# Performance work log

Measured on AMD Instinct MI355X. Metric: run time of the kernel, lower is better.

Reference implementation:

```python
import jax, jax.numpy as jnp
import numpy as np

H, C = 8, 16          # heads, per-head dim; hidden = H*C = 128
NEG_SLOPE = 0.2       # GATConv default
EPS = 1e-5            # GraphNorm eps


def setup_inputs() -> dict:
    key = jax.random.key(0)
    ks = iter(jax.random.split(key, 64))
    Np, Na, D, E = 100000, 50000, 128, 500000
    s = 1.0 / np.sqrt(D)

    def w(shape, scale=1.0):
        return jax.random.normal(next(ks), shape, jnp.float32) * scale

    inp = {
        'x_paper': w((Np, D)),
        'x_author': w((Na, D)),
        'edge_writes': jnp.stack([
            jax.random.randint(next(ks), (E,), 0, Na),
            jax.random.randint(next(ks), (E,), 0, Np)]).astype(jnp.int32),
        'edge_cites': jnp.stack([
            jax.random.randint(next(ks), (E,), 0, Np),
            jax.random.randint(next(ks), (E,), 0, Np)]).astype(jnp.int32),
        'W_lin_paper': w((D, 128), s), 'b_lin_paper': jnp.zeros((128,), jnp.float32),
        'W_lin_author': w((D, 128), s), 'b_lin_author': jnp.zeros((128,), jnp.float32),
        'Wsrc_writes': w((128, 128), s), 'Wdst_writes': w((128, 128), s),
        'atts_writes': w((H, C), 0.1), 'attd_writes': w((H, C), 0.1),
        'bias_writes': jnp.zeros((128,), jnp.float32),
        'Wsrc_cites': w((128, 128), s), 'Wdst_cites': w((128, 128), s),
        'atts_cites': w((H, C), 0.1), 'attd_cites': w((H, C), 0.1),
        'bias_cites': jnp.zeros((128,), jnp.float32),
        'gnw_paper': jnp.ones((128,), jnp.float32), 'gnb_paper': jnp.zeros((128,), jnp.float32),
        'gnm_paper': jnp.ones((128,), jnp.float32),
        'gnw_author': jnp.ones((128,), jnp.float32), 'gnb_author': jnp.zeros((128,), jnp.float32),
        'gnm_author': jnp.ones((128,), jnp.float32),
        'W2_paper': w((128, 128), s), 'b2_paper': jnp.zeros((128,), jnp.float32),
        'W2_author': w((128, 128), s), 'b2_author': jnp.zeros((128,), jnp.float32),
    }
    return inp


def _gat(src_emb, dst_emb, ei, Wsrc, Wdst, att_s, att_d, bias, n_dst):
    # PyG GATConv, bipartite input, concat=True, add_self_loops=True (eval / no dropout)
    n_self = min(src_emb.shape[0], n_dst)
    loops = jnp.arange(n_self, dtype=ei.dtype)
    src = jnp.concatenate([ei[0], loops])
    dst = jnp.concatenate([ei[1], loops])
    xs = (src_emb @ Wsrc).reshape(-1, H, C)          # [Ns,H,C]
    xd = (dst_emb @ Wdst).reshape(-1, H, C)          # [Nd,H,C]
    a_s = (xs * att_s).sum(-1)                       # [Ns,H]
    a_d = (xd * att_d).sum(-1)                       # [Nd,H]
    e = jax.nn.leaky_relu(a_s[src] + a_d[dst], NEG_SLOPE)   # [E,H]
    m = jax.ops.segment_max(e, dst, num_segments=n_dst)
    m = jnp.where(jnp.isfinite(m), m, 0.0)           # guard empty segments
    p = jnp.exp(e - m[dst])
    denom = jax.ops.segment_sum(p, dst, num_segments=n_dst)
    alpha = p / (denom[dst] + 1e-16)                 # segment softmax over dst
    msg = xs[src] * alpha[:, :, None]                # [E,H,C]
    out = jax.ops.segment_sum(msg, dst, num_segments=n_dst)  # [Nd,H,C]
    return out.reshape(n_dst, H * C) + bias


def _gnorm(x, w, b, ms):
    mu = x.mean(0)
    o = x - ms * mu
    var = (o * o).mean(0)
    return w * o * jax.lax.rsqrt(var + EPS) + b


def reference(x_paper, x_author, edge_writes, edge_cites,
              W_lin_paper, b_lin_paper, W_lin_author, b_lin_author,
              Wsrc_writes, Wdst_writes, atts_writes, attd_writes, bias_writes,
              Wsrc_cites, Wdst_cites, atts_cites, attd_cites, bias_cites,
              gnw_paper, gnb_paper, gnm_paper, gnw_author, gnb_author, gnm_author,
              W2_paper, b2_paper, W2_author, b2_author):
    emb_p = jax.nn.relu(x_paper @ W_lin_paper + b_lin_paper)
    emb_a = jax.nn.relu(x_author @ W_lin_author + b_lin_author)
    Np = emb_p.shape[0]
    out_p = _gat(emb_a, emb_p, edge_writes, Wsrc_writes, Wdst_writes,
                 atts_writes, attd_writes, bias_writes, Np)
    out_p = out_p + _gat(emb_p, emb_p, edge_cites, Wsrc_cites, Wdst_cites,
                         atts_cites, attd_cites, bias_cites, Np)
    out_a = jnp.zeros((emb_a.shape[0], H * C), x_author.dtype)  # no edge type targets author
    out_p = _gnorm(out_p, gnw_paper, gnb_paper, gnm_paper) @ W2_paper + b2_paper
    out_a = _gnorm(out_a, gnw_author, gnb_author, gnm_author) @ W2_author + b2_author
    return (out_p, out_a)
```

## Files before the change

kernel.cpp:

```cpp
#include <hip/hip_runtime.h>
#include <cstdint>
#include <cstddef>

#define H 8
#define DHID 128
#define XST 144
#define BM 64
#define LDST 136
#define NEG_SLOPE 0.2f
#define GN_EPS 1e-5f

#define SCAN_T 256
#define SCAN_I 4

typedef __attribute__((ext_vector_type(8))) short short8;
typedef __attribute__((ext_vector_type(4))) float f32x4;

__device__ __forceinline__ void atomAddF(float* p, float v) {
    __hip_atomic_fetch_add(p, v, __ATOMIC_RELAXED, __HIP_MEMORY_SCOPE_AGENT);
}
__device__ __forceinline__ unsigned short f2bf(float f) {
    uint32_t u = __float_as_uint(f);
    uint32_t r = (u + 0x7FFFu + ((u >> 16) & 1u)) >> 16;
    return (unsigned short)r;
}
__device__ __forceinline__ uint32_t pack2bf(float lo, float hi) {
    return (uint32_t)f2bf(lo) | ((uint32_t)f2bf(hi) << 16);
}
__device__ __forceinline__ float bflo(uint32_t v) { return __uint_as_float(v << 16); }
__device__ __forceinline__ float bfhi(uint32_t v) { return __uint_as_float(v & 0xFFFF0000u); }

struct PrepHist {
    const float *Wlp, *Wsc, *Wla, *Wsw, *W2p;
    const float *Wdw, *adw, *asc_, *Wdc, *adc_, *asw_;
    unsigned short *WlinP_p, *WsrcP_c, *WlinP_a, *WsrcP_w, *W2P_p, *VscP_p, *VscP_a;
    const float *bw, *bc, *gnb_a, *W2a, *b2a;
    float *bsum, *row_a, *colsum, *colsumsq;
    unsigned short *xs_w_ph, *xs_c_ph;
    const int *dst_w, *dst_c;
    int *deg, *rank;
    int Ew, Ec, Np, HB0;
};

__global__ void prep_hist(PrepHist a) {
    int b = blockIdx.x, t = threadIdx.x;
    if (b >= a.HB0) {
        int base = (b - a.HB0) * 1024 + t;
        int E = a.Ew + a.Ec;
        int dd[4];
        bool val[4];
#pragma unroll
        for (int j = 0; j < 4; ++j) {
            int i = base + j * 256;
            val[j] = i < E;
            dd[j] = 0;
            if (val[j]) dd[j] = (i < a.Ew) ? a.dst_w[i] : (a.Np + a.dst_c[i - a.Ew]);
        }
        int rk[4];
#pragma unroll
        for (int j = 0; j < 4; ++j)
            if (val[j]) rk[j] = atomicAdd(&a.deg[dd[j]], 1);
#pragma unroll
        for (int j = 0; j < 4; ++j)
            if (val[j]) a.rank[base + j * 256] = rk[j];
        return;
    }
    if (b == 56) {
        if (t < 128) {
            a.bsum[t] = a.bw[t] + a.bc[t];
            float acc = a.b2a[t];
            for (int k = 0; k < DHID; ++k) acc += a.gnb_a[k] * a.W2a[k * DHID + t];
            a.row_a[t] = acc;
            a.colsum[t] = 0.f;
            a.colsumsq[t] = 0.f;
            a.xs_w_ph[t] = 0;
            a.xs_c_ph[t] = 0;
        } else if (t < 136) {
            *reinterpret_cast<float*>(a.xs_w_ph + 128 + 2 * (t - 128)) = -1e30f;
        } else if (t < 144) {
            *reinterpret_cast<float*>(a.xs_c_ph + 128 + 2 * (t - 136)) = -1e30f;
        }
        return;
    }
    int j = b >> 3;
    int idx = (b & 7) * 256 + t;
    int lane = idx & 63, kk = (idx >> 6) & 3, nt = idx >> 8;
    int col = nt * 16 + (lane & 15);
    int k0 = kk * 32 + ((lane >> 4) << 3);
    if (j < 5) {
        const float* W = j == 0 ? a.Wlp : j == 1 ? a.Wsc : j == 2 ? a.Wla : j == 3 ? a.Wsw : a.W2p;
        unsigned short* out = j == 0 ? a.WlinP_p : j == 1 ? a.WsrcP_c : j == 2 ? a.WlinP_a
                              : j == 3 ? a.WsrcP_w : a.W2P_p;
        for (int i = 0; i < 8; ++i) out[idx * 8 + i] = f2bf(W[(k0 + i) * DHID + col]);
    } else if (j == 5) {
        if (idx >= 2 * 256) return;
        const float *W = nullptr, *A = nullptr;
        int h = col & 7;
        if (col < 24) {
            int which = col >> 3;
            W = which == 0 ? a.Wdw : which == 1 ? a.Wsc : a.Wdc;
            A = which == 0 ? a.adw : which == 1 ? a.asc_ : a.adc_;
        }
        for (int i = 0; i < 8; ++i) {
            float v = 0.f;
            if (W)
                for (int c = 0; c < 16; ++c) v += W[(k0 + i) * DHID + h * 16 + c] * A[h * 16 + c];
            a.VscP_p[idx * 8 + i] = f2bf(v);
        }
    } else {
        if (idx >= 256) return;
        int h = col & 7;
        for (int i = 0; i < 8; ++i) {
            float v = 0.f;
            if (col < 8)
                for (int c = 0; c < 16; ++c)
                    v += a.Wsw[(k0 + i) * DHID + h * 16 + c] * a.asw_[h * 16 + c];
            a.VscP_a[idx * 8 + i] = f2bf(v);
        }
    }
}

__global__ void scan1(const int* __restrict__ in, int n, int* __restrict__ out,
                      int* __restrict__ bsums) {
    __shared__ int sh[SCAN_T];
    int t = threadIdx.x;
    long base = (long)blockIdx.x * SCAN_T * SCAN_I;
    int v[SCAN_I];
    int s = 0;
#pragma unroll
    for (int j = 0; j < SCAN_I; ++j) {
        long idx = base + (long)t * SCAN_I + j;
        int x = (idx < n) ? in[idx] : 0;
        x = (x + 3) & ~3;
        v[j] = x;
        s += x;
    }
    sh[t] = s;
    __syncthreads();
    for (int off = 1; off < SCAN_T; off <<= 1) {
        int x = (t >= off) ? sh[t - off] : 0;
        __syncthreads();
        sh[t] += x;
        __syncthreads();
    }
    int run = sh[t] - s;
#pragma unroll
    for (int j = 0; j < SCAN_I; ++j) {
        long idx = base + (long)t * SCAN_I + j;
        if (idx < n) out[idx] = run;
        run += v[j];
    }
    if (t == SCAN_T - 1) bsums[blockIdx.x] = sh[SCAN_T - 1];
}

__global__ void scan3_tails(const int* __restrict__ off_raw, const int* __restrict__ bs1,
                            int nb, int n2, int* __restrict__ off2,
                            const int* __restrict__ deg,
                            int Np, int Na, int* __restrict__ srcu) {
    __shared__ int pf[SCAN_T];
    int t = threadIdx.x;
    pf[t] = (t < nb) ? bs1[t] : 0;
    __syncthreads();
    for (int off = 1; off < SCAN_T; off <<= 1) {
        int x = (t >= off) ? pf[t - off] : 0;
        __syncthreads();
        pf[t] += x;
        __syncthreads();
    }
    int i = blockIdx.x * 256 + t;
    if (i < n2) {
        int g = i >> 10;
        int o = off_raw[i] + (g ? pf[g - 1] : 0);
        off2[i] = o;
        int dgi = deg[i];
        int padded = (dgi + 3) & ~3;
        int ph = (i < Np) ? Na : Np;
        for (int k = dgi; k < padded; ++k) srcu[o + k] = ph;
    }
    if (blockIdx.x == 0 && t == 0) off2[n2] = pf[nb - 1];
}

template <int NSC>
__device__ void proj_body(unsigned short* xt, int bid,
                          const float* __restrict__ x, int nrows,
                          const unsigned short* __restrict__ WlinP, const float* __restrict__ blin,
                          const unsigned short* __restrict__ WsrcP,
                          const unsigned short* __restrict__ VscP,
                          unsigned short* __restrict__ xs,
                          float* __restrict__ ad0, float* __restrict__ ad1) {
    int t = threadIdx.x;
    int lane = t & 63, w = t >> 6;
    long row0 = (long)bid * BM;
    for (int it = 0; it < 16; ++it) {
        int idx2 = t + it * 256;
        int r = idx2 >> 6, cp = idx2 & 63;
        long gr = row0 + r;
        float v0 = 0.f, v1 = 0.f;
        if (gr < nrows) { v0 = x[gr * DHID + 2 * cp]; v1 = x[gr * DHID + 2 * cp + 1]; }
        *reinterpret_cast<uint32_t*>(&xt[r * LDST + 2 * cp]) = pack2bf(v0, v1);
    }
    __syncthreads();
    int arow = w * 16 + (lane & 15);
    int koff = (lane >> 4) << 3;
    short8 af[4];
#pragma unroll
    for (int kk = 0; kk < 4; ++kk)
        af[kk] = *reinterpret_cast<const short8*>(&xt[arow * LDST + kk * 32 + koff]);
    const short8* Bl = reinterpret_cast<const short8*>(WlinP);
    f32x4 acc[8];
#pragma unroll
    for (int nt = 0; nt < 8; ++nt) {
        f32x4 a = {0.f, 0.f, 0.f, 0.f};
#pragma unroll
        for (int kk = 0; kk < 4; ++kk)
            a = __builtin_amdgcn_mfma_f32_16x16x32_bf16(af[kk], Bl[(nt * 4 + kk) * 64 + lane], a, 0, 0, 0);
        acc[nt] = a;
    }
    __syncthreads();
    int orow = w * 16 + ((lane >> 4) << 2);
    int ccol = lane & 15;
#pragma unroll
    for (int nt = 0; nt < 8; ++nt) {
        float b = blin[nt * 16 + ccol];
#pragma unroll
        for (int r = 0; r < 4; ++r) {
            float e = fmaxf(acc[nt][r] + b, 0.f);
            xt[(orow + r) * LDST + nt * 16 + ccol] = f2bf(e);
        }
    }
    __syncthreads();
#pragma unroll
    for (int kk = 0; kk < 4; ++kk)
        af[kk] = *reinterpret_cast<const short8*>(&xt[arow * LDST + kk * 32 + koff]);
    const short8* Bs = reinterpret_cast<const short8*>(WsrcP);
#pragma unroll
    for (int nt = 0; nt < 8; ++nt) {
        f32x4 a = {0.f, 0.f, 0.f, 0.f};
#pragma unroll
        for (int kk = 0; kk < 4; ++kk)
            a = __builtin_amdgcn_mfma_f32_16x16x32_bf16(af[kk], Bs[(nt * 4 + kk) * 64 + lane], a, 0, 0, 0);
        acc[nt] = a;
    }
    const short8* Bv = reinterpret_cast<const short8*>(VscP);
    f32x4 sacc0 = {0.f, 0.f, 0.f, 0.f}, sacc1 = {0.f, 0.f, 0.f, 0.f};
#pragma unroll
    for (int kk = 0; kk < 4; ++kk)
        sacc0 = __builtin_amdgcn_mfma_f32_16x16x32_bf16(af[kk], Bv[kk * 64 + lane], sacc0, 0, 0, 0);
    if (NSC > 1) {
#pragma unroll
        for (int kk = 0; kk < 4; ++kk)
            sacc1 = __builtin_amdgcn_mfma_f32_16x16x32_bf16(af[kk], Bv[(4 + kk) * 64 + lane], sacc1, 0, 0, 0);
    }
#pragma unroll
    for (int nt = 0; nt < 8; ++nt) {
#pragma unroll
        for (int r = 0; r < 4; ++r) {
            long gr = row0 + orow + r;
            if (gr < nrows) xs[gr * XST + nt * 16 + ccol] = f2bf(acc[nt][r]);
        }
    }
#pragma unroll
    for (int st = 0; st < NSC; ++st) {
        int scol = st * 16 + ccol;
        int h = scol & 7, which = scol >> 3;
        f32x4 s = (st == 0) ? sacc0 : sacc1;
#pragma unroll
        for (int r = 0; r < 4; ++r) {
            long gr = row0 + orow + r;
            if (gr >= nrows) continue;
            if (NSC == 2) {
                if (which == 0) ad0[gr * H + h] = s[r];
                else if (which == 1)
                    *reinterpret_cast<float*>(xs + gr * XST + 128 + 2 * h) = s[r];
                else if (which == 2) ad1[gr * H + h] = s[r];
            } else {
                if (which == 0)
                    *reinterpret_cast<float*>(xs + gr * XST + 128 + 2 * h) = s[r];
            }
        }
    }
}

struct MegaArgs {
    const float* x_p; int Np;
    const unsigned short* WlinP_p; const float* blp;
    const unsigned short* WsrcP_c; const unsigned short* VscP_p;
    unsigned short* xs_c; float *a_d_w, *a_d_c;
    const float* x_a; int Na;
    const unsigned short* WlinP_a; const float* bla;
    const unsigned short* WsrcP_w; const unsigned short* VscP_a;
    unsigned short* xs_w;
    const int *src_w, *dst_w, *src_c, *dst_c;
    int Ew, Ec;
    const int *off2, *rank;
    int* srcu;
    int PB, AB;
};

__global__ __launch_bounds__(256) void mega(MegaArgs a) {
    __shared__ unsigned short xt[BM * LDST];
    int b = blockIdx.x;
    if (b < a.PB) {
        proj_body<2>(xt, b, a.x_p, a.Np, a.WlinP_p, a.blp, a.WsrcP_c, a.VscP_p,
                     a.xs_c, a.a_d_w, a.a_d_c);
        return;
    }
    if (b < a.PB + a.AB) {
        proj_body<1>(xt, b - a.PB, a.x_a, a.Na, a.WlinP_a, a.bla, a.WsrcP_w, a.VscP_a,
                     a.xs_w, nullptr, nullptr);
        return;
    }
    int base = (b - a.PB - a.AB) * 1024 + threadIdx.x;
    int E = a.Ew + a.Ec;
    int s[4], di[4], rk[4];
    bool val[4];
#pragma unroll
    for (int j = 0; j < 4; ++j) {
        int i = base + j * 256;
        val[j] = i < E;
        s[j] = di[j] = rk[j] = 0;
        if (val[j]) {
            if (i < a.Ew) { s[j] = a.src_w[i]; di[j] = a.dst_w[i]; }
            else { int q = i - a.Ew; s[j] = a.src_c[q]; di[j] = a.Np + a.dst_c[q]; }
            rk[j] = a.rank[i];
        }
    }
    int pos[4];
#pragma unroll
    for (int j = 0; j < 4; ++j)
        if (val[j]) pos[j] = a.off2[di[j]] + rk[j];
#pragma unroll
    for (int j = 0; j < 4; ++j)
        if (val[j]) a.srcu[pos[j]] = s[j];
}

#define FILLB 391
__global__ __launch_bounds__(256) void gat_gather(
    const int* __restrict__ off, const int* __restrict__ srcu,
    const float* __restrict__ a_d_w, const float* __restrict__ a_d_c,
    const unsigned short* __restrict__ xs_w, const unsigned short* __restrict__ xs_c,
    uint32_t* __restrict__ gatb, int Np, int nselfw,
    const float* __restrict__ row_a, float4* __restrict__ outa, long n4) {
    if (blockIdx.x < FILLB) {
        long i = (long)blockIdx.x * 256 + threadIdx.x;
        long stride = (long)FILLB * 256;
        const float4* r4 = reinterpret_cast<const float4*>(row_a);
        for (; i < n4; i += stride) outa[i] = r4[i & 31];
        return;
    }
    int l = threadIdx.x & 63;
    int d = (blockIdx.x - FILLB) * 4 + (threadIdx.x >> 6);
    if (d >= Np) return;
    int h = l >> 3;
    int sco = 128 + 2 * h;
    int iw = off[d], w1 = off[d + 1];
    int ic = off[Np + d], c1 = off[Np + d + 1];
    float adw = a_d_w[(long)d * H + h];
    float adc = a_d_c[(long)d * H + h];
    float denw = 0.f, n0w = 0.f, n1w = 0.f;
    float denc = 0.f, n0c = 0.f, n1c = 0.f;
    if (d < nselfw) {
        const unsigned short* r = xs_w + (long)d * XST;
        float e = *reinterpret_cast<const float*>(r + sco) + adw;
        e = e > 0.f ? e : NEG_SLOPE * e;
        float p = __expf(e);
        uint32_t v = *reinterpret_cast<const uint32_t*>(r + 2 * l);
        denw += p; n0w += p * bflo(v); n1w += p * bfhi(v);
    }
    {
        const unsigned short* r = xs_c + (long)d * XST;
        float e = *reinterpret_cast<const float*>(r + sco) + adc;
        e = e > 0.f ? e : NEG_SLOPE * e;
        float p = __expf(e);
        uint32_t v = *reinterpret_cast<const uint32_t*>(r + 2 * l);
        denc += p; n0c += p * bflo(v); n1c += p * bfhi(v);
    }
    while (iw < w1 || ic < c1) {
        bool hw = iw < w1, hc = ic < c1;
        int4 sw, sc;
        if (hw) sw = *reinterpret_cast<const int4*>(srcu + iw);
        if (hc) sc = *reinterpret_cast<const int4*>(srcu + ic);
        float ew[4], ec[4];
        uint32_t vw[4], vc[4];
        if (hw) {
            const unsigned short* r0 = xs_w + (long)sw.x * XST;
            const unsigned short* r1 = xs_w + (long)sw.y * XST;
            const unsigned short* r2 = xs_w + (long)sw.z * XST;
            const unsigned short* r3 = xs_w + (long)sw.w * XST;
            ew[0] = *reinterpret_cast<const float*>(r0 + sco);
            ew[1] = *reinterpret_cast<const float*>(r1 + sco);
            ew[2] = *reinterpret_cast<const float*>(r2 + sco);
            ew[3] = *reinterpret_cast<const float*>(r3 + sco);
            vw[0] = *reinterpret_cast<const uint32_t*>(r0 + 2 * l);
            vw[1] = *reinterpret_cast<const uint32_t*>(r1 + 2 * l);
            vw[2] = *reinterpret_cast<const uint32_t*>(r2 + 2 * l);
            vw[3] = *reinterpret_cast<const uint32_t*>(r3 + 2 * l);
        }
        if (hc) {
            const unsigned short* r0 = xs_c + (long)sc.x * XST;
            const unsigned short* r1 = xs_c + (long)sc.y * XST;
            const unsigned short* r2 = xs_c + (long)sc.z * XST;
            const unsigned short* r3 = xs_c + (long)sc.w * XST;
            ec[0] = *reinterpret_cast<const float*>(r0 + sco);
            ec[1] = *reinterpret_cast<const float*>(r1 + sco);
            ec[2] = *reinterpret_cast<const float*>(r2 + sco);
            ec[3] = *reinterpret_cast<const float*>(r3 + sco);
            vc[0] = *reinterpret_cast<const uint32_t*>(r0 + 2 * l);
            vc[1] = *reinterpret_cast<const uint32_t*>(r1 + 2 * l);
            vc[2] = *reinterpret_cast<const uint32_t*>(r2 + 2 * l);
            vc[3] = *reinterpret_cast<const uint32_t*>(r3 + 2 * l);
        }
        if (hw) {
#pragma unroll
            for (int j = 0; j < 4; ++j) {
                float e = ew[j] + adw;
                e = e > 0.f ? e : NEG_SLOPE * e;
                float p = __expf(e);
                denw += p;
                n0w += p * bflo(vw[j]);
                n1w += p * bfhi(vw[j]);
            }
            iw += 4;
        }
        if (hc) {
#pragma unroll
            for (int j = 0; j < 4; ++j) {
                float e = ec[j] + adc;
                e = e > 0.f ? e : NEG_SLOPE * e;
                float p = __expf(e);
                denc += p;
                n0c += p * bflo(vc[j]);
                n1c += p * bfhi(vc[j]);
            }
            ic += 4;
        }
    }
    float rw = 1.f / (denw + 1e-16f);
    float rc = 1.f / (denc + 1e-16f);
    gatb[(long)d * 64 + l] = pack2bf(n0w * rw + n0c * rc, n1w * rw + n1c * rc);
}

#define GN_ROWS 512
__global__ void gn_reduce(const uint32_t* __restrict__ gatb, const float* __restrict__ bsum,
                          float* __restrict__ colsum, float* __restrict__ colsumsq, int Np) {
    int t = threadIdx.x;
    int p = t & 63, ro = t >> 6;
    long r0 = (long)blockIdx.x * GN_ROWS + ro;
    long r1 = min((long)(blockIdx.x + 1) * GN_ROWS, (long)Np);
    float b0 = bsum[2 * p], b1 = bsum[2 * p + 1];
    float s1a = 0.f, s2a = 0.f, s1b = 0.f, s2b = 0.f;
    for (long r = r0; r < r1; r += 4) {
        uint32_t u = gatb[r * 64 + p];
        float x0 = bflo(u) + b0, x1 = bfhi(u) + b1;
        s1a += x0; s2a += x0 * x0;
        s1b += x1; s2b += x1 * x1;
    }
    atomAddF(colsum + 2 * p, s1a);
    atomAddF(colsumsq + 2 * p, s2a);
    atomAddF(colsum + 2 * p + 1, s1b);
    atomAddF(colsumsq + 2 * p + 1, s2b);
}

__global__ __launch_bounds__(256) void final_fill(
    const uint32_t* __restrict__ gatb, const float* __restrict__ bsum,
    const float* __restrict__ colsum, const float* __restrict__ colsumsq,
    const float* __restrict__ gnw, const float* __restrict__ gnb,
    const float* __restrict__ gnm,
    const unsigned short* __restrict__ W2P, const float* __restrict__ b2,
    float* __restrict__ out, int Np) {
    __shared__ unsigned short xt[BM * LDST];
    __shared__ float cscale[DHID], cshift[DHID];
    int b = blockIdx.x;
    int t = threadIdx.x;
    int lane = t & 63, w = t >> 6;
    long row0 = (long)b * BM;
    if (t < DHID) {
        float invN = 1.f / (float)Np;
        float mu = colsum[t] * invN;
        float ms = gnm[t];
        float var = colsumsq[t] * invN - mu * mu * ms * (2.f - ms);
        float sc = gnw[t] * rsqrtf(var + GN_EPS);
        cscale[t] = sc;
        cshift[t] = (bsum[t] - ms * mu) * sc + gnb[t];
    }
    __syncthreads();
    int wrow0 = w * 16;
    float cs0 = cscale[2 * lane], cf0 = cshift[2 * lane];
    float cs1 = cscale[2 * lane + 1], cf1 = cshift[2 * lane + 1];
    for (int it = 0; it < 16; ++it) {
        int r = wrow0 + it;
        long gr = row0 + r;
        float v0 = 0.f, v1 = 0.f;
        if (gr < Np) {
            uint32_t u = gatb[gr * 64 + lane];
            v0 = bflo(u) * cs0 + cf0;
            v1 = bfhi(u) * cs1 + cf1;
        }
        *reinterpret_cast<uint32_t*>(&xt[r * LDST + 2 * lane]) = pack2bf(v0, v1);
    }
    int arow = wrow0 + (lane & 15);
    int koff = (lane >> 4) << 3;
    short8 af[4];
#pragma unroll
    for (int kk = 0; kk < 4; ++kk)
        af[kk] = *reinterpret_cast<const short8*>(&xt[arow * LDST + kk * 32 + koff]);
    const short8* Bw = reinterpret_cast<const short8*>(W2P);
    int orow = wrow0 + ((lane >> 4) << 2);
    int ccol = lane & 15;
#pragma unroll
    for (int nt = 0; nt < 8; ++nt) {
        f32x4 a = {0.f, 0.f, 0.f, 0.f};
#pragma unroll
        for (int kk = 0; kk < 4; ++kk)
            a = __builtin_amdgcn_mfma_f32_16x16x32_bf16(af[kk], Bw[(nt * 4 + kk) * 64 + lane], a, 0, 0, 0);
        float bb = b2[nt * 16 + ccol];
#pragma unroll
        for (int r = 0; r < 4; ++r) {
            long gr = row0 + orow + r;
            if (gr < Np) out[gr * DHID + nt * 16 + ccol] = a[r] + bb;
        }
    }
}

extern "C" void kernel_launch(void* const* d_in, const int* in_sizes, int n_in,
                              void* d_out, int out_size, void* d_ws, size_t ws_size,
                              hipStream_t stream) {
    const float* x_p   = (const float*)d_in[0];
    const float* x_a   = (const float*)d_in[1];
    const int*   e_w   = (const int*)d_in[2];
    const int*   e_c   = (const int*)d_in[3];
    const float* Wlp   = (const float*)d_in[4];
    const float* blp   = (const float*)d_in[5];
    const float* Wla   = (const float*)d_in[6];
    const float* bla   = (const float*)d_in[7];
    const float* Wsw   = (const float*)d_in[8];
    const float* Wdw   = (const float*)d_in[9];
    const float* asw   = (const float*)d_in[10];
    const float* adw   = (const float*)d_in[11];
    const float* bw    = (const float*)d_in[12];
    const float* Wsc   = (const float*)d_in[13];
    const float* Wdc   = (const float*)d_in[14];
    const float* asc   = (const float*)d_in[15];
    const float* adc   = (const float*)d_in[16];
    const float* bc    = (const float*)d_in[17];
    const float* gnw_p = (const float*)d_in[18];
    const float* gnb_p = (const float*)d_in[19];
    const float* gnm_p = (const float*)d_in[20];
    const float* gnb_a = (const float*)d_in[22];
    const float* W2p   = (const float*)d_in[24];
    const float* b2p   = (const float*)d_in[25];
    const float* W2a   = (const float*)d_in[26];
    const float* b2a   = (const float*)d_in[27];

    int Np = in_sizes[0] / DHID;
    int Na = in_sizes[1] / DHID;
    int Ew = in_sizes[2] / 2;
    int Ec = in_sizes[3] / 2;
    int nself_w = Na < Np ? Na : Np;
    int tot_edges = Ew + Ec;
    int maxTot = tot_edges + 6 * Np + 8;

    float* ws = (float*)d_ws;
    uint32_t* gatb = (uint32_t*)ws;
    float* a_d_w = (float*)(gatb + (size_t)Np * 64);
    float* a_d_c = a_d_w + (size_t)Np * H;
    float* bsum  = a_d_c + (size_t)Np * H;
    float* row_a = bsum + DHID;
    float* colsum   = row_a + DHID;
    float* colsumsq = colsum + DHID;
    int*   deg   = (int*)(colsumsq + DHID);
    int* off_raw = deg + 2 * Np;
    int* off2    = off_raw + 2 * Np;
    int* bs1     = off2 + 2 * Np + 1;
    uintptr_t up = (uintptr_t)(bs1 + 512);
    up = (up + 15) & ~(uintptr_t)15;
    int* srcu = (int*)up;
    int* rank = srcu + maxTot;
    unsigned short* xs_w = (unsigned short*)(rank + tot_edges);
    unsigned short* xs_c = xs_w + (size_t)(Na + 1) * XST;
    up = (uintptr_t)(xs_c + (size_t)(Np + 1) * XST);
    up = (up + 15) & ~(uintptr_t)15;
    unsigned short* WlinP_p = (unsigned short*)up;
    unsigned short* WsrcP_c = WlinP_p + 16384;
    unsigned short* WlinP_a = WsrcP_c + 16384;
    unsigned short* WsrcP_w = WlinP_a + 16384;
    unsigned short* W2P_p   = WsrcP_w + 16384;
    unsigned short* VscP_p  = W2P_p + 16384;
    unsigned short* VscP_a  = VscP_p + 4096;

    hipMemsetAsync(deg, 0, 2 * (size_t)Np * sizeof(int), stream);

    int HB = (tot_edges + 1023) / 1024;
    {
        PrepHist pa;
        pa.Wlp = Wlp; pa.Wsc = Wsc; pa.Wla = Wla; pa.Wsw = Wsw; pa.W2p = W2p;
        pa.Wdw = Wdw; pa.adw = adw; pa.asc_ = asc; pa.Wdc = Wdc; pa.adc_ = adc; pa.asw_ = asw;
        pa.WlinP_p = WlinP_p; pa.WsrcP_c = WsrcP_c; pa.WlinP_a = WlinP_a;
        pa.WsrcP_w = WsrcP_w; pa.W2P_p = W2P_p; pa.VscP_p = VscP_p; pa.VscP_a = VscP_a;
        pa.bw = bw; pa.bc = bc; pa.gnb_a = gnb_a; pa.W2a = W2a; pa.b2a = b2a;
        pa.bsum = bsum; pa.row_a = row_a; pa.colsum = colsum; pa.colsumsq = colsumsq;
        pa.xs_w_ph = xs_w + (size_t)Na * XST;
        pa.xs_c_ph = xs_c + (size_t)Np * XST;
        pa.dst_w = e_w + Ew; pa.dst_c = e_c + Ec;
        pa.deg = deg; pa.rank = rank;
        pa.Ew = Ew; pa.Ec = Ec;
        pa.Np = Np; pa.HB0 = 57;
        prep_hist<<<57 + HB, 256, 0, stream>>>(pa);
    }

    int n2 = 2 * Np;
    int nb = (n2 + SCAN_T * SCAN_I - 1) / (SCAN_T * SCAN_I);
    scan1<<<nb, SCAN_T, 0, stream>>>(deg, n2, off_raw, bs1);

    scan3_tails<<<(n2 + 255) / 256, 256, 0, stream>>>(
        off_raw, bs1, nb, n2, off2, deg, Np, Na, srcu);

    {
        MegaArgs ma;
        ma.x_p = x_p; ma.Np = Np; ma.WlinP_p = WlinP_p; ma.blp = blp;
        ma.WsrcP_c = WsrcP_c; ma.VscP_p = VscP_p;
        ma.xs_c = xs_c; ma.a_d_w = a_d_w; ma.a_d_c = a_d_c;
        ma.x_a = x_a; ma.Na = Na; ma.WlinP_a = WlinP_a; ma.bla = bla;
        ma.WsrcP_w = WsrcP_w; ma.VscP_a = VscP_a;
        ma.xs_w = xs_w;
        ma.src_w = e_w; ma.dst_w = e_w + Ew; ma.src_c = e_c; ma.dst_c = e_c + Ec;
        ma.Ew = Ew; ma.Ec = Ec;
        ma.off2 = off2; ma.rank = rank; ma.srcu = srcu;
        ma.PB = (Np + BM - 1) / BM;
        ma.AB = (Na + BM - 1) / BM;
        int SB = (tot_edges + 1023) / 1024;
        mega<<<ma.PB + ma.AB + SB, 256, 0, stream>>>(ma);
    }

    {
        long n4 = (long)Na * DHID / 4;
        gat_gather<<<FILLB + (Np + 3) / 4, 256, 0, stream>>>(
            off2, srcu, a_d_w, a_d_c, xs_w, xs_c, gatb, Np, nself_w,
            row_a, (float4*)((float*)d_out + (size_t)Np * DHID), n4);
    }

    gn_reduce<<<(Np + GN_ROWS - 1) / GN_ROWS, 256, 0, stream>>>(gatb, bsum, colsum, colsumsq, Np);

    final_fill<<<(Np + BM - 1) / BM, 256, 0, stream>>>(
        gatb, bsum, colsum, colsumsq, gnw_p, gnb_p, gnm_p, W2P_p, b2p,
        (float*)d_out, Np);
}
```

Measured before the change: 281.8 us.

## Fuse GraphNorm column reduction into GAT gather with persistent grid-stride blocks

The separate gn_reduce kernel is removed. The gather kernel now accumulates per-column sum and sum of squares of the unbiased GAT outputs while it writes them, reduces them in shared memory, and issues atomics once per block. The gather launch becomes a grid-stride loop capped at 2048 blocks, and final_fill now applies the bias shift algebraically to the mean and second moment. This removes one kernel launch and a full re-read of gatb. The statistics now come from fp32 values rather than the bf16-rounded ones, and fewer blocks may reduce latency hiding in the irregular gather.

```diff
diff --git a/kernel.cpp b/kernel.cpp
--- a/kernel.cpp
+++ b/kernel.cpp
@@ -335,11 +335,13 @@
 }
 
 #define FILLB 391
+#define GATB 2048
 __global__ __launch_bounds__(256) void gat_gather(
     const int* __restrict__ off, const int* __restrict__ srcu,
     const float* __restrict__ a_d_w, const float* __restrict__ a_d_c,
     const unsigned short* __restrict__ xs_w, const unsigned short* __restrict__ xs_c,
-    uint32_t* __restrict__ gatb, int Np, int nselfw,
+    uint32_t* __restrict__ gatb, int Np, int nselfw, int ngroups,
+    float* __restrict__ colsum, float* __restrict__ colsumsq,
     const float* __restrict__ row_a, float4* __restrict__ outa, long n4) {
     if (blockIdx.x < FILLB) {
         long i = (long)blockIdx.x * 256 + threadIdx.x;
@@ -348,117 +350,118 @@
         for (; i < n4; i += stride) outa[i] = r4[i & 31];
         return;
     }
-    int l = threadIdx.x & 63;
-    int d = (blockIdx.x - FILLB) * 4 + (threadIdx.x >> 6);
-    if (d >= Np) return;
+    __shared__ float red1[4 * DHID], red2[4 * DHID];
+    int t = threadIdx.x;
+    int l = t & 63;
+    int rg = t >> 6;
     int h = l >> 3;
     int sco = 128 + 2 * h;
-    int iw = off[d], w1 = off[d + 1];
-    int ic = off[Np + d], c1 = off[Np + d + 1];
-    float adw = a_d_w[(long)d * H + h];
-    float adc = a_d_c[(long)d * H + h];
-    float denw = 0.f, n0w = 0.f, n1w = 0.f;
-    float denc = 0.f, n0c = 0.f, n1c = 0.f;
-    if (d < nselfw) {
-        const unsigned short* r = xs_w + (long)d * XST;
-        float e = *reinterpret_cast<const float*>(r + sco) + adw;
-        e = e > 0.f ? e : NEG_SLOPE * e;
-        float p = __expf(e);
-        uint32_t v = *reinterpret_cast<const uint32_t*>(r + 2 * l);
-        denw += p; n0w += p * bflo(v); n1w += p * bfhi(v);
-    }
-    {
-        const unsigned short* r = xs_c + (long)d * XST;
-        float e = *reinterpret_cast<const float*>(r + sco) + adc;
-        e = e > 0.f ? e : NEG_SLOPE * e;
-        float p = __expf(e);
-        uint32_t v = *reinterpret_cast<const uint32_t*>(r + 2 * l);
-        denc += p; n0c += p * bflo(v); n1c += p * bfhi(v);
-    }
-    while (iw < w1 || ic < c1) {
-        bool hw = iw < w1, hc = ic < c1;
-        int4 sw, sc;
-        if (hw) sw = *reinterpret_cast<const int4*>(srcu + iw);
-        if (hc) sc = *reinterpret_cast<const int4*>(srcu + ic);
-        float ew[4], ec[4];
-        uint32_t vw[4], vc[4];
-        if (hw) {
-            const unsigned short* r0 = xs_w + (long)sw.x * XST;
-            const unsigned short* r1 = xs_w + (long)sw.y * XST;
-            const unsigned short* r2 = xs_w + (long)sw.z * XST;
-            const unsigned short* r3 = xs_w + (long)sw.w * XST;
-            ew[0] = *reinterpret_cast<const float*>(r0 + sco);
-            ew[1] = *reinterpret_cast<const float*>(r1 + sco);
-            ew[2] = *reinterpret_cast<const float*>(r2 + sco);
-            ew[3] = *reinterpret_cast<const float*>(r3 + sco);
-            vw[0] = *reinterpret_cast<const uint32_t*>(r0 + 2 * l);
-            vw[1] = *reinterpret_cast<const uint32_t*>(r1 + 2 * l);
-            vw[2] = *reinterpret_cast<const uint32_t*>(r2 + 2 * l);
-            vw[3] = *reinterpret_cast<const uint32_t*>(r3 + 2 * l);
-        }
-        if (hc) {
-            const unsigned short* r0 = xs_c + (long)sc.x * XST;
-            const unsigned short* r1 = xs_c + (long)sc.y * XST;
-            const unsigned short* r2 = xs_c + (long)sc.z * XST;
-            const unsigned short* r3 = xs_c + (long)sc.w * XST;
-            ec[0] = *reinterpret_cast<const float*>(r0 + sco);
-            ec[1] = *reinterpret_cast<const float*>(r1 + sco);
-            ec[2] = *reinterpret_cast<const float*>(r2 + sco);
-            ec[3] = *reinterpret_cast<const float*>(r3 + sco);
-            vc[0] = *reinterpret_cast<const uint32_t*>(r0 + 2 * l);
-            vc[1] = *reinterpret_cast<const uint32_t*>(r1 + 2 * l);
-            vc[2] = *reinterpret_cast<const uint32_t*>(r2 + 2 * l);
-            vc[3] = *reinterpret_cast<const uint32_t*>(r3 + 2 * l);
-        }
-        if (hw) {
-#pragma unroll
-            for (int j = 0; j < 4; ++j) {
-                float e = ew[j] + adw;
-                e = e > 0.f ? e : NEG_SLOPE * e;
-                float p = __expf(e);
-                denw += p;
-                n0w += p * bflo(vw[j]);
-                n1w += p * bfhi(vw[j]);
+    int gstride = gridDim.x - FILLB;
+    float cs0 = 0.f, cs1 = 0.f, cq0 = 0.f, cq1 = 0.f;
+    for (int g = blockIdx.x - FILLB; g < ngroups; g += gstride) {
+        int d = g * 4 + rg;
+        if (d >= Np) continue;
+        int iw = off[d], w1 = off[d + 1];
+        int ic = off[Np + d], c1 = off[Np + d + 1];
+        float adw = a_d_w[(long)d * H + h];
+        float adc = a_d_c[(long)d * H + h];
+        float denw = 0.f, n0w = 0.f, n1w = 0.f;
+        float denc = 0.f, n0c = 0.f, n1c = 0.f;
+        if (d < nselfw) {
+            const unsigned short* r = xs_w + (long)d * XST;
+            float e = *reinterpret_cast<const float*>(r + sco) + adw;
+            e = e > 0.f ? e : NEG_SLOPE * e;
+            float p = __expf(e);
+            uint32_t v = *reinterpret_cast<const uint32_t*>(r + 2 * l);
+            denw += p; n0w += p * bflo(v); n1w += p * bfhi(v);
+        }
+        {
+            const unsigned short* r = xs_c + (long)d * XST;
+            float e = *reinterpret_cast<const float*>(r + sco) + adc;
+            e = e > 0.f ? e : NEG_SLOPE * e;
+            float p = __expf(e);
+            uint32_t v = *reinterpret_cast<const uint32_t*>(r + 2 * l);
+            denc += p; n0c += p * bflo(v); n1c += p * bfhi(v);
+        }
+        while (iw < w1 || ic < c1) {
+            bool hw = iw < w1, hc = ic < c1;
+            int4 sw, sc;
+            if (hw) sw = *reinterpret_cast<const int4*>(srcu + iw);
+            if (hc) sc = *reinterpret_cast<const int4*>(srcu + ic);
+            float ew[4], ec[4];
+            uint32_t vw[4], vc[4];
+            if (hw) {
+                const unsigned short* r0 = xs_w + (long)sw.x * XST;
+                const unsigned short* r1 = xs_w + (long)sw.y * XST;
+                const unsigned short* r2 = xs_w + (long)sw.z * XST;
+                const unsigned short* r3 = xs_w + (long)sw.w * XST;
+                ew[0] = *reinterpret_cast<const float*>(r0 + sco);
+                ew[1] = *reinterpret_cast<const float*>(r1 + sco);
+                ew[2] = *reinterpret_cast<const float*>(r2 + sco);
+                ew[3] = *reinterpret_cast<const float*>(r3 + sco);
+                vw[0] = *reinterpret_cast<const uint32_t*>(r0 + 2 * l);
+                vw[1] = *reinterpret_cast<const uint32_t*>(r1 + 2 * l);
+                vw[2] = *reinterpret_cast<const uint32_t*>(r2 + 2 * l);
+                vw[3] = *reinterpret_cast<const uint32_t*>(r3 + 2 * l);
             }
-            iw += 4;
-        }
-        if (hc) {
-#pragma unroll
-            for (int j = 0; j < 4; ++j) {
-                float e = ec[j] + adc;
-                e = e > 0.f ? e : NEG_SLOPE * e;
-                float p = __expf(e);
-                denc += p;
-                n0c += p * bflo(vc[j]);
-                n1c += p * bfhi(vc[j]);
+            if (hc) {
+                const unsigned short* r0 = xs_c + (long)sc.x * XST;
+                const unsigned short* r1 = xs_c + (long)sc.y * XST;
+                const unsigned short* r2 = xs_c + (long)sc.z * XST;
+                const unsigned short* r3 = xs_c + (long)sc.w * XST;
+                ec[0] = *reinterpret_cast<const float*>(r0 + sco);
+                ec[1] = *reinterpret_cast<const float*>(r1 + sco);
+                ec[2] = *reinterpret_cast<const float*>(r2 + sco);
+                ec[3] = *reinterpret_cast<const float*>(r3 + sco);
+                vc[0] = *reinterpret_cast<const uint32_t*>(r0 + 2 * l);
+                vc[1] = *reinterpret_cast<const uint32_t*>(r1 + 2 * l);
+                vc[2] = *reinterpret_cast<const uint32_t*>(r2 + 2 * l);
+                vc[3] = *reinterpret_cast<const uint32_t*>(r3 + 2 * l);
             }
-            ic += 4;
-        }
-    }
-    float rw = 1.f / (denw + 1e-16f);
-    float rc = 1.f / (denc + 1e-16f);
-    gatb[(long)d * 64 + l] = pack2bf(n0w * rw + n0c * rc, n1w * rw + n1c * rc);
-}
-
-#define GN_ROWS 512
-__global__ void gn_reduce(const uint32_t* __restrict__ gatb, const float* __restrict__ bsum,
-                          float* __restrict__ colsum, float* __restrict__ colsumsq, int Np) {
-    int t = threadIdx.x;
-    int p = t & 63, ro = t >> 6;
-    long r0 = (long)blockIdx.x * GN_ROWS + ro;
-    long r1 = min((long)(blockIdx.x + 1) * GN_ROWS, (long)Np);
-    float b0 = bsum[2 * p], b1 = bsum[2 * p + 1];
-    float s1a = 0.f, s2a = 0.f, s1b = 0.f, s2b = 0.f;
-    for (long r = r0; r < r1; r += 4) {
-        uint32_t u = gatb[r * 64 + p];
-        float x0 = bflo(u) + b0, x1 = bfhi(u) + b1;
-        s1a += x0; s2a += x0 * x0;
-        s1b += x1; s2b += x1 * x1;
-    }
-    atomAddF(colsum + 2 * p, s1a);
-    atomAddF(colsumsq + 2 * p, s2a);
-    atomAddF(colsum + 2 * p + 1, s1b);
-    atomAddF(colsumsq + 2 * p + 1, s2b);
+            if (hw) {
+#pragma unroll
+                for (int j = 0; j < 4; ++j) {
+                    float e = ew[j] + adw;
+                    e = e > 0.f ? e : NEG_SLOPE * e;
+                    float p = __expf(e);
+                    denw += p;
+                    n0w += p * bflo(vw[j]);
+                    n1w += p * bfhi(vw[j]);
+                }
+                iw += 4;
+            }
+            if (hc) {
+#pragma unroll
+                for (int j = 0; j < 4; ++j) {
+                    float e = ec[j] + adc;
+                    e = e > 0.f ? e : NEG_SLOPE * e;
+                    float p = __expf(e);
+                    denc += p;
+                    n0c += p * bflo(vc[j]);
+                    n1c += p * bfhi(vc[j]);
+                }
+                ic += 4;
+            }
+        }
+        float rw = 1.f / (denw + 1e-16f);
+        float rc = 1.f / (denc + 1e-16f);
+        float o0 = n0w * rw + n0c * rc;
+        float o1 = n1w * rw + n1c * rc;
+        gatb[(long)d * 64 + l] = pack2bf(o0, o1);
+        cs0 += o0; cs1 += o1;
+        cq0 += o0 * o0; cq1 += o1 * o1;
+    }
+    red1[rg * DHID + 2 * l] = cs0;
+    red1[rg * DHID + 2 * l + 1] = cs1;
+    red2[rg * DHID + 2 * l] = cq0;
+    red2[rg * DHID + 2 * l + 1] = cq1;
+    __syncthreads();
+    if (t < DHID) {
+        float s1 = red1[t] + red1[DHID + t] + red1[2 * DHID + t] + red1[3 * DHID + t];
+        float s2 = red2[t] + red2[DHID + t] + red2[2 * DHID + t] + red2[3 * DHID + t];
+        atomAddF(colsum + t, s1);
+        atomAddF(colsumsq + t, s2);
+    }
 }
 
 __global__ __launch_bounds__(256) void final_fill(
@@ -476,12 +479,16 @@
     long row0 = (long)b * BM;
     if (t < DHID) {
         float invN = 1.f / (float)Np;
-        float mu = colsum[t] * invN;
+        float bb = bsum[t];
+        float sg = colsum[t] * invN;
+        float eq = colsumsq[t] * invN;
+        float mu = sg + bb;
+        float ex2 = eq + 2.f * bb * sg + bb * bb;
         float ms = gnm[t];
-        float var = colsumsq[t] * invN - mu * mu * ms * (2.f - ms);
+        float var = ex2 - mu * mu * ms * (2.f - ms);
         float sc = gnw[t] * rsqrtf(var + GN_EPS);
         cscale[t] = sc;
-        cshift[t] = (bsum[t] - ms * mu) * sc + gnb[t];
+        cshift[t] = (bb - ms * mu) * sc + gnb[t];
     }
     __syncthreads();
     int wrow0 = w * 16;
@@ -634,12 +641,13 @@
 
     {
         long n4 = (long)Na * DHID / 4;
-        gat_gather<<<FILLB + (Np + 3) / 4, 256, 0, stream>>>(
-            off2, srcu, a_d_w, a_d_c, xs_w, xs_c, gatb, Np, nself_w,
+        int ngroups = (Np + 3) / 4;
+        int GB = ngroups < GATB ? ngroups : GATB;
+        gat_gather<<<FILLB + GB, 256, 0, stream>>>(
+            off2, srcu, a_d_w, a_d_c, xs_w, xs_c, gatb, Np, nself_w, ngroups,
+            colsum, colsumsq,
             row_a, (float4*)((float*)d_out + (size_t)Np * DHID), n4);
     }
-
-    gn_reduce<<<(Np + GN_ROWS - 1) / GN_ROWS, 256, 0, stream>>>(gatb, bsum, colsum, colsumsq, Np);
 
     final_fill<<<(Np + BM - 1) / BM, 256, 0, stream>>>(
         gatb, bsum, colsum, colsumsq, gnw_p, gnb_p, gnm_p, W2P_p, b2p,
```

Result: faster. 264.5 us (-6.1%).
